# Performance work log

Hardware: AMD Instinct MI355X
Metric: run time of the kernel (lower is better)

Reference implementation:

```python
import jax, jax.numpy as jnp
import numpy as np
from jax import lax

STRIDE = 16
ANCHOR_BASE = 16
PRE_NMS = 6000
POST_NMS = 2000
NMS_THRESH = 0.7


def _generate_anchors(base_size=16, ratios=(0.5, 1.0, 2.0), scales=(8, 16, 32)):
    w = h = float(base_size)
    x_ctr = 0.5 * (w - 1)
    y_ctr = 0.5 * (h - 1)
    size = w * h
    anchors = []
    for r in ratios:
        ws = np.round(np.sqrt(size / r))
        hs = np.round(ws * r)
        for s in scales:
            wss, hss = ws * s, hs * s
            anchors.append([x_ctr - 0.5 * (wss - 1), y_ctr - 0.5 * (hss - 1),
                            x_ctr + 0.5 * (wss - 1), y_ctr + 0.5 * (hss - 1)])
    return np.array(anchors, dtype=np.float32)  # [9,4]


def _all_anchors(width, height, stride):
    base = _generate_anchors(ANCHOR_BASE)  # [A,4]
    sx = np.arange(width, dtype=np.float32) * stride
    gy, gx = np.meshgrid(np.arange(height, dtype=np.float32) * stride, sx, indexing='ij')
    shifts = np.stack([gx.ravel(), gy.ravel(), gx.ravel(), gy.ravel()], axis=1)  # [K,4] h-major
    return jnp.asarray((shifts[:, None, :] + base[None, :, :]).reshape(-1, 4))  # [K*A,4]


def setup_inputs() -> dict:
    key = jax.random.key(0)
    k1, k2 = jax.random.split(key)
    H = W = 64
    bbox_deltas = jax.random.normal(k1, (1, 36, H, W), dtype=jnp.float32)
    scores = jax.random.uniform(k2, (1, 2, 9 * H, W), dtype=jnp.float32)
    return {"bbox_deltas": bbox_deltas, "scores": scores, "im_w": 1024, "im_h": 1024}


def reference(bbox_deltas, scores, im_w, im_h):
    H, W = bbox_deltas.shape[2], bbox_deltas.shape[3]
    # fg scores: reshape [1,2,9H,W] -> [1,18,H,W], take channels 9:18
    sc = scores.reshape(1, 18, H, W)[:, 9:, :, :].transpose(0, 2, 3, 1).reshape(-1)
    dl = bbox_deltas.transpose(0, 2, 3, 1).reshape(-1, 4)
    anchors = _all_anchors(W, H, STRIDE)

    # bbox_transform_inv (decode)
    aw = anchors[:, 2] - anchors[:, 0] + 1.0
    ah = anchors[:, 3] - anchors[:, 1] + 1.0
    acx = anchors[:, 0] + 0.5 * aw
    acy = anchors[:, 1] + 0.5 * ah
    pcx = dl[:, 0] * aw + acx
    pcy = dl[:, 1] * ah + acy
    pw = jnp.exp(dl[:, 2]) * aw
    ph = jnp.exp(dl[:, 3]) * ah
    x1 = jnp.clip(pcx - 0.5 * pw, 0.0, im_w - 1.0)
    y1 = jnp.clip(pcy - 0.5 * ph, 0.0, im_h - 1.0)
    x2 = jnp.clip(pcx + 0.5 * pw, 0.0, im_w - 1.0)
    y2 = jnp.clip(pcy + 0.5 * ph, 0.0, im_h - 1.0)
    props = jnp.stack([x1, y1, x2, y2], axis=1)

    # min-size filter
    thresh = 16.0 * (float(im_h) / float(im_w))
    keep_f = ((x2 - x1 + 1.0) >= thresh) & ((y2 - y1 + 1.0) >= thresh)
    sc_m = jnp.where(keep_f, sc, -jnp.inf)

    # pre-NMS top-k by score
    top_sc, idx = lax.top_k(sc_m, PRE_NMS)
    top_p = props[idx]  # [PRE_NMS,4], sorted by score desc
    valid = jnp.isfinite(top_sc)

    # pairwise IoU (with +1 box convention, as in py_cpu_nms)
    bx1, by1, bx2, by2 = top_p[:, 0], top_p[:, 1], top_p[:, 2], top_p[:, 3]
    areas = (bx2 - bx1 + 1.0) * (by2 - by1 + 1.0)
    iw = jnp.maximum(jnp.minimum(bx2[:, None], bx2[None, :]) - jnp.maximum(bx1[:, None], bx1[None, :]) + 1.0, 0.0)
    ih = jnp.maximum(jnp.minimum(by2[:, None], by2[None, :]) - jnp.maximum(by1[:, None], by1[None, :]) + 1.0, 0.0)
    inter = iw * ih
    iou = inter / (areas[:, None] + areas[None, :] - inter)
    sup = iou > NMS_THRESH  # [N,N]

    ar = jnp.arange(PRE_NMS)

    def body(i, keep):
        row = sup[i] & keep[i] & (ar > i)
        return keep & (~row)

    keep = lax.fori_loop(0, PRE_NMS, body, valid)

    # take first POST_NMS kept (in score order), scatter into fixed-size output
    rank = jnp.cumsum(keep.astype(jnp.int32)) - 1
    sel = keep & (rank < POST_NMS)
    dst = jnp.where(sel, rank, POST_NMS)  # invalid rows dumped into slot POST_NMS
    out_b = jnp.zeros((POST_NMS + 1, 4), dtype=jnp.float32).at[dst].set(
        jnp.where(sel[:, None], top_p, 0.0))[:POST_NMS]
    out_s = jnp.zeros((POST_NMS + 1,), dtype=jnp.float32).at[dst].set(
        jnp.where(sel, top_sc, 0.0))[:POST_NMS]
    blob = jnp.concatenate([jnp.zeros((POST_NMS, 1), dtype=jnp.float32), out_b], axis=1)
    return blob, out_s[:, None]
```

## Files before the change

kernel.cpp:

```cpp
#include <hip/hip_runtime.h>
#include <math.h>

typedef unsigned int u32;
typedef unsigned long long u64;

#define NANCH   36864
#define PRE     6000
#define POST    2000
#define NWORDS  94

#define OFF_PROPS   ((size_t)0)
#define OFF_SV      ((size_t)589824)
#define OFF_SORTED  ((size_t)884736)
#define OFF_SEL     ((size_t)932864)
#define OFF_MASK    ((size_t)1227776)
#define OFF_CTRL    ((size_t)5739776)
#define OFF_H1      ((size_t)5740032)
#define OFF_INVALW  ((size_t)5744384)
#define OFF_KEEPW   ((size_t)5745152)
#define ZERO_BYTES  ((size_t)(256 + 4352 + 768))

__device__ __constant__ float BA[9][4] = {
  {-84.f,-40.f,99.f,55.f},   {-176.f,-88.f,191.f,103.f}, {-360.f,-184.f,375.f,199.f},
  {-56.f,-56.f,71.f,71.f},   {-120.f,-120.f,135.f,135.f},{-248.f,-248.f,263.f,263.f},
  {-36.f,-80.f,51.f,95.f},   {-80.f,-168.f,95.f,183.f},  {-168.f,-344.f,183.f,359.f}};

__device__ __forceinline__ u32 key_bin(u32 key) {
  if (key < 0xBF000000u) return 0u;
  u32 b = ((key >> 13) - 0x5F800u) + 1u;
  return b > 1024u ? 1024u : b;
}

__global__ void decode_k(const float* __restrict__ deltas, const float* __restrict__ scores,
                         const int* __restrict__ imw_p, const int* __restrict__ imh_p,
                         float4* __restrict__ props, u64* __restrict__ sortvals,
                         u32* __restrict__ h1) {
  #pragma clang fp contract(off)
  int i = blockIdx.x * 256 + threadIdx.x;
  if (i >= NANCH) return;
  int a = i % 9;
  int pix = i / 9;
  int x = pix & 63, y = pix >> 6;

  float sc = scores[(9 + a) * 4096 + pix];
  float d0 = deltas[(a * 4 + 0) * 4096 + pix];
  float d1 = deltas[(a * 4 + 1) * 4096 + pix];
  float d2 = deltas[(a * 4 + 2) * 4096 + pix];
  float d3 = deltas[(a * 4 + 3) * 4096 + pix];

  float gx = (float)(x * 16), gy = (float)(y * 16);
  float ax1 = gx + BA[a][0], ay1 = gy + BA[a][1];
  float ax2 = gx + BA[a][2], ay2 = gy + BA[a][3];
  float aw = ax2 - ax1 + 1.0f, ah = ay2 - ay1 + 1.0f;
  float acx = ax1 + 0.5f * aw, acy = ay1 + 0.5f * ah;

  float pcx = d0 * aw + acx;
  float pcy = d1 * ah + acy;
  float pw = (float)exp((double)d2) * aw;
  float ph = (float)exp((double)d3) * ah;

  float imw1 = (float)imw_p[0] - 1.0f, imh1 = (float)imh_p[0] - 1.0f;
  float x1 = fminf(fmaxf(pcx - 0.5f * pw, 0.0f), imw1);
  float y1 = fminf(fmaxf(pcy - 0.5f * ph, 0.0f), imh1);
  float x2 = fminf(fmaxf(pcx + 0.5f * pw, 0.0f), imw1);
  float y2 = fminf(fmaxf(pcy + 0.5f * ph, 0.0f), imh1);
  props[i] = make_float4(x1, y1, x2, y2);

  float thresh = 16.0f * ((float)imh_p[0] / (float)imw_p[0]);
  bool keep = (x2 - x1 + 1.0f >= thresh) && (y2 - y1 + 1.0f >= thresh);
  u32 key = keep ? (__float_as_uint(sc) | 0x80000000u) : 0u;
  sortvals[i] = ((u64)key << 32) | (u64)(0xFFFFFFFFu - (u32)i);
  u32 bin = key_bin(key);
  if (bin) atomicAdd(&h1[bin], 1u);
}

__global__ void scan_k(const u32* __restrict__ h1, u32* __restrict__ ctrl) {
  int l = threadIdx.x;
  u32 loc[16], suf[16];
  #pragma unroll
  for (int k = 0; k < 16; ++k) loc[k] = h1[1 + l * 16 + k];
  u32 acc = 0;
  #pragma unroll
  for (int k = 15; k >= 0; --k) { acc += loc[k]; suf[k] = acc; }
  u32 sfx = acc;
  for (int off = 1; off < 64; off <<= 1) {
    u32 o = __shfl_down(sfx, off);
    if (l + off < 64) sfx += o;
  }
  u32 S_above = sfx - acc;
  u64 mball = __ballot(suf[0] + S_above >= (u32)PRE);
  if (mball == 0ULL) { if (l == 0) ctrl[0] = 0u; return; }
  int L = 63 - __builtin_clzll(mball);
  if (l == L) {
    int kk = 0;
    for (int k = 15; k >= 0; --k)
      if (suf[k] + S_above >= (u32)PRE) { kk = k; break; }
    ctrl[0] = (u32)(1 + 16 * L + kk);
  }
}

__global__ void compact_k(const u64* __restrict__ sv, u32* __restrict__ ctrl,
                          u64* __restrict__ sel) {
  int i = blockIdx.x * 256 + threadIdx.x;
  if (i >= NANCH) return;
  u32 chosen = ctrl[0];
  u64 v = sv[i];
  if (key_bin((u32)(v >> 32)) >= chosen) {
    u32 p = atomicAdd(&ctrl[6], 1u);
    sel[p] = v;
  }
}

__global__ void rank_k(const u64* __restrict__ sel, const u32* __restrict__ ctrl,
                       u64* __restrict__ sorted, u64* __restrict__ invalw) {
  __shared__ u64 sj[256];
  u32 n = ctrl[6];
  int i = blockIdx.x * 256 + threadIdx.x;
  if ((u32)(blockIdx.x * 256) >= n) return;
  u64 vi = ((u32)i < n) ? sel[i] : 0ULL;
  u32 cnt = 0;
  for (u32 jb = 0; jb < n; jb += 256) {
    __syncthreads();
    if (jb + threadIdx.x < n) sj[threadIdx.x] = sel[jb + threadIdx.x];
    __syncthreads();
    u32 m = min(256u, n - jb);
    #pragma unroll 8
    for (u32 j = 0; j < m; ++j) cnt += (u32)(sj[j] > vi);
  }
  if ((u32)i < n && cnt < (u32)PRE) {
    sorted[cnt] = vi;
    if ((u32)(vi >> 32) == 0u)
      atomicOr((unsigned long long*)&invalw[cnt >> 6], 1ULL << (cnt & 63));
  }
}

__global__ void mask_k(const u64* __restrict__ sorted, const float4* __restrict__ props,
                       u64* __restrict__ mask) {
  #pragma clang fp contract(off)
  __shared__ float4 cb[64];
  int jb = blockIdx.x;
  if (jb < (int)blockIdx.y) return;
  int i = blockIdx.y * 64 + threadIdx.x;
  int jj = jb * 64 + threadIdx.x;
  float4 cc = make_float4(0.f, 0.f, 0.f, 0.f);
  if (jj < PRE) {
    u64 v = sorted[jj];
    cc = props[0xFFFFu - ((u32)v & 0xFFFFu)];
  }
  cb[threadIdx.x] = cc;
  __syncthreads();
  if (i >= PRE) return;
  u64 vi = sorted[i];
  float4 b = props[0xFFFFu - ((u32)vi & 0xFFFFu)];
  float ai = (b.z - b.x + 1.0f) * (b.w - b.y + 1.0f);
  u64 bits = 0ULL;
  int jmax = min(64, PRE - jb * 64);
  for (int j = 0; j < jmax; ++j) {
    float4 c = cb[j];
    float aj = (c.z - c.x + 1.0f) * (c.w - c.y + 1.0f);
    float iw = fmaxf(fminf(b.z, c.z) - fmaxf(b.x, c.x) + 1.0f, 0.0f);
    float ih = fmaxf(fminf(b.w, c.w) - fmaxf(b.y, c.y) + 1.0f, 0.0f);
    float inter = iw * ih;
    float iou = inter / (ai + aj - inter);
    bits |= ((u64)(iou > 0.7f)) << j;
  }
  mask[(size_t)i * NWORDS + jb] = bits;
}

__device__ __forceinline__ u64 rl64(u64 v, int lane) {
  u32 lo = (u32)__builtin_amdgcn_readlane((int)(u32)v, lane);
  u32 hi = (u32)__builtin_amdgcn_readlane((int)(u32)(v >> 32), lane);
  return ((u64)hi << 32) | (u64)lo;
}
__device__ __forceinline__ u64 rfl64(u64 v) {
  u32 lo = (u32)__builtin_amdgcn_readfirstlane((int)(u32)v);
  u32 hi = (u32)__builtin_amdgcn_readfirstlane((int)(u32)(v >> 32));
  return ((u64)hi << 32) | (u64)lo;
}

__global__ void __launch_bounds__(1024) nms_scan_k(const u64* __restrict__ mask,
                                                   const u64* __restrict__ invalw,
                                                   u64* __restrict__ keepw) {
  __shared__ u64 Lrem[NWORDS];
  __shared__ u64 Ldiag[64];
  __shared__ u64 Lkeep;
  __shared__ int Lstop;
  __shared__ int Llast;
  const int t = threadIdx.x;
  const int g = t >> 7;
  const int w = t & 127;
  const bool loader = (w < NWORDS);
  if (t < NWORDS) Lrem[t] = invalw[t];
  if (t == 0) { Lstop = 0; Llast = NWORDS - 1; }
  u64 rv = 0;
  u64 B0[8], B1[8], B2[8];
  int kept = 0;
  __syncthreads();

#define ISSUE(bb, BUF) \
  if ((bb) < NWORDS && loader) { \
    u64 st_ = Lrem[(bb)]; \
    const int row0_ = (bb) * 64 + g * 8; \
    const u64* pp_ = mask + (size_t)row0_ * NWORDS + w; \
    _Pragma("unroll") \
    for (int j = 0; j < 8; ++j) { \
      bool ok_ = (w >= (bb)) && (row0_ + j < PRE) && !((st_ >> (g * 8 + j)) & 1ULL); \
      BUF[j] = ok_ ? pp_[(size_t)j * NWORDS] : 0ULL; \
    } \
  }

#define STEP(bb, BUF) { \
    if (w == (bb)) {                      \
      atomicOr((u32*)&Lrem[(bb)], (u32)rv); \
      atomicOr(((u32*)&Lrem[(bb)]) + 1, (u32)(rv >> 32)); \
      _Pragma("unroll") \
      for (int j = 0; j < 8; ++j) Ldiag[g * 8 + j] = BUF[j]; \
    } \
    if ((bb) + 3 < NWORDS && w == (bb) + 3) {   \
      atomicOr((u32*)&Lrem[(bb) + 3], (u32)rv); \
      atomicOr(((u32*)&Lrem[(bb) + 3]) + 1, (u32)(rv >> 32)); \
    } \
    __syncthreads();                      \
    if (t < 64) { \
      u64 dgl = Ldiag[t]; \
      u64 avail = ~rfl64(Lrem[(bb)]);     \
      u64 kb = 0; \
      while (avail) { \
        int i_ = __builtin_ctzll(avail); \
        kb |= 1ULL << i_; \
        u64 di_ = rl64(dgl, i_); \
        avail &= ~di_ & ~((2ULL << i_) - 1ULL);  \
      } \
      if (t == 0) { \
        keepw[(bb)] = kb; \
        Lkeep = kb; \
        kept += (int)__popcll(kb); \
        if (kept >= POST) { Lstop = 1; Llast = (bb); } \
      } \
    } \
    __syncthreads();                      \
    { \
      u64 kb_ = Lkeep; \
      const int base_ = g * 8; \
      _Pragma("unroll") \
      for (int j = 0; j < 8; ++j) { \
        u64 k_ = (kb_ >> (base_ + j)) & 1ULL; \
        rv |= (0ULL - k_) & BUF[j]; \
      } \
    } \
    ISSUE((bb) + 3, BUF)                  \
    if (Lstop) break; }

  ISSUE(0, B0)
  ISSUE(1, B1)
  ISSUE(2, B2)
  for (int bb = 0; bb < NWORDS; bb += 3) {
    STEP(bb, B0)
    if (bb + 1 < NWORDS) STEP(bb + 1, B1)
    if (bb + 2 < NWORDS) STEP(bb + 2, B2)
  }
#undef ISSUE
#undef STEP

  __syncthreads();
  int last = Llast;
  for (int w2 = t; w2 < NWORDS; w2 += 1024)
    if (w2 > last) keepw[w2] = 0ULL;
}

__global__ void outscatter_k(const u64* __restrict__ keepw, const u64* __restrict__ sorted,
                             const float4* __restrict__ props, float* __restrict__ out) {
  __shared__ u64 wl[NWORDS];
  __shared__ u32 pre[NWORDS];
  int t = threadIdx.x;
  for (int i = t; i < 12000; i += 1024) out[i] = 0.0f;
  if (t < NWORDS) wl[t] = keepw[t];
  __syncthreads();
  if (t == 0) {
    u32 run = 0;
    for (int w = 0; w < NWORDS; ++w) { pre[w] = run; run += (u32)__popcll(wl[w]); }
  }
  __syncthreads();
  for (int i = t; i < PRE; i += 1024) {
    int w = i >> 6;
    u64 word = wl[w];
    if ((word >> (i & 63)) & 1ULL) {
      u32 rank = pre[w] + (u32)__popcll(word & ((1ULL << (i & 63)) - 1ULL));
      if (rank < POST) {
        u64 v = sorted[i];
        float4 b = props[0xFFFFu - ((u32)v & 0xFFFFu)];
        out[rank * 5 + 1] = b.x;
        out[rank * 5 + 2] = b.y;
        out[rank * 5 + 3] = b.z;
        out[rank * 5 + 4] = b.w;
        out[10000 + rank] = __uint_as_float((u32)(v >> 32) & 0x7FFFFFFFu);
      }
    }
  }
}

extern "C" void kernel_launch(void* const* d_in, const int* in_sizes, int n_in,
                              void* d_out, int out_size, void* d_ws, size_t ws_size,
                              hipStream_t stream) {
  const float* deltas = (const float*)d_in[0];
  const float* scores = (const float*)d_in[1];
  const int* imw = (const int*)d_in[2];
  const int* imh = (const int*)d_in[3];
  char* ws = (char*)d_ws;

  float4* props   = (float4*)(ws + OFF_PROPS);
  u64*    svals   = (u64*)(ws + OFF_SV);
  u64*    sorted  = (u64*)(ws + OFF_SORTED);
  u64*    sel     = (u64*)(ws + OFF_SEL);
  u64*    maskb   = (u64*)(ws + OFF_MASK);
  u32*    ctrl    = (u32*)(ws + OFF_CTRL);
  u32*    h1      = (u32*)(ws + OFF_H1);
  u64*    invalw  = (u64*)(ws + OFF_INVALW);
  u64*    keepw   = (u64*)(ws + OFF_KEEPW);

  hipMemsetAsync(ws + OFF_CTRL, 0, ZERO_BYTES, stream);

  decode_k<<<144, 256, 0, stream>>>(deltas, scores, imw, imh, props, svals, h1);
  scan_k<<<1, 64, 0, stream>>>(h1, ctrl);
  compact_k<<<144, 256, 0, stream>>>(svals, ctrl, sel);
  rank_k<<<144, 256, 0, stream>>>(sel, ctrl, sorted, invalw);

  dim3 mgrid(NWORDS, NWORDS);
  mask_k<<<mgrid, 64, 0, stream>>>(sorted, props, maskb);

  nms_scan_k<<<1, 1024, 0, stream>>>(maskb, invalw, keepw);
  outscatter_k<<<1, 1024, 0, stream>>>(keepw, sorted, props, (float*)d_out);
}
```

Measured before the change: 334.6 us.

## Replace single-block NMS scan with multi-block pipelined scan over transposed mask

The mask kernel now writes the IoU suppression bitmask column-major (transposed, padded rows), so each column of 64 boxes is contiguous. The single 1024-thread NMS scan is replaced by 47 single-wavefront blocks, each owning two consecutive 64-box words. Each block prefetches its column of mask words, then spin-waits on keep-words that earlier blocks publish through global memory as a value/complement pair, and ORs in the suppression. The serial dependency shrinks to a cross-block handoff of one word, and the many block-wide barriers go away. The cost is agent-scope polling latency, reliance on all blocks being co-resident, and the loss of the early stop once enough boxes are kept.

```diff
diff --git a/kernel.cpp b/kernel.cpp
--- a/kernel.cpp
+++ b/kernel.cpp
@@ -8,17 +8,20 @@
 #define PRE     6000
 #define POST    2000
 #define NWORDS  94
+#define NST     47
+#define ROWSP   6016
 
 #define OFF_PROPS   ((size_t)0)
 #define OFF_SV      ((size_t)589824)
 #define OFF_SORTED  ((size_t)884736)
 #define OFF_SEL     ((size_t)932864)
-#define OFF_MASK    ((size_t)1227776)
-#define OFF_CTRL    ((size_t)5739776)
-#define OFF_H1      ((size_t)5740032)
-#define OFF_INVALW  ((size_t)5744384)
-#define OFF_KEEPW   ((size_t)5745152)
-#define ZERO_BYTES  ((size_t)(256 + 4352 + 768))
+#define OFF_MASKT   ((size_t)1227776)
+#define OFF_CTRL    ((size_t)5751808)
+#define OFF_H1      ((size_t)5752064)
+#define OFF_INVALW  ((size_t)5756416)
+#define OFF_KBP     ((size_t)5757184)
+#define OFF_KBN     ((size_t)5757952)
+#define ZERO_BYTES  ((size_t)(256 + 4352 + 768 + 768 + 768))
 
 __device__ __constant__ float BA[9][4] = {
   {-84.f,-40.f,99.f,55.f},   {-176.f,-88.f,191.f,103.f}, {-360.f,-184.f,375.f,199.f},
@@ -135,7 +138,7 @@
 }
 
 __global__ void mask_k(const u64* __restrict__ sorted, const float4* __restrict__ props,
-                       u64* __restrict__ mask) {
+                       u64* __restrict__ maskT) {
   #pragma clang fp contract(off)
   __shared__ float4 cb[64];
   int jb = blockIdx.x;
@@ -164,7 +167,7 @@
     float iou = inter / (ai + aj - inter);
     bits |= ((u64)(iou > 0.7f)) << j;
   }
-  mask[(size_t)i * NWORDS + jb] = bits;
+  maskT[(size_t)jb * ROWSP + i] = bits;
 }
 
 __device__ __forceinline__ u64 rl64(u64 v, int lane) {
@@ -172,100 +175,77 @@
   u32 hi = (u32)__builtin_amdgcn_readlane((int)(u32)(v >> 32), lane);
   return ((u64)hi << 32) | (u64)lo;
 }
-__device__ __forceinline__ u64 rfl64(u64 v) {
-  u32 lo = (u32)__builtin_amdgcn_readfirstlane((int)(u32)v);
-  u32 hi = (u32)__builtin_amdgcn_readfirstlane((int)(u32)(v >> 32));
-  return ((u64)hi << 32) | (u64)lo;
-}
-
-__global__ void __launch_bounds__(1024) nms_scan_k(const u64* __restrict__ mask,
-                                                   const u64* __restrict__ invalw,
-                                                   u64* __restrict__ keepw) {
-  __shared__ u64 Lrem[NWORDS];
-  __shared__ u64 Ldiag[64];
-  __shared__ u64 Lkeep;
-  __shared__ int Lstop;
-  __shared__ int Llast;
-  const int t = threadIdx.x;
-  const int g = t >> 7;
-  const int w = t & 127;
-  const bool loader = (w < NWORDS);
-  if (t < NWORDS) Lrem[t] = invalw[t];
-  if (t == 0) { Lstop = 0; Llast = NWORDS - 1; }
-  u64 rv = 0;
-  u64 B0[8], B1[8], B2[8];
-  int kept = 0;
-  __syncthreads();
-
-#define ISSUE(bb, BUF) \
-  if ((bb) < NWORDS && loader) { \
-    u64 st_ = Lrem[(bb)]; \
-    const int row0_ = (bb) * 64 + g * 8; \
-    const u64* pp_ = mask + (size_t)row0_ * NWORDS + w; \
-    _Pragma("unroll") \
-    for (int j = 0; j < 8; ++j) { \
-      bool ok_ = (w >= (bb)) && (row0_ + j < PRE) && !((st_ >> (g * 8 + j)) & 1ULL); \
-      BUF[j] = ok_ ? pp_[(size_t)j * NWORDS] : 0ULL; \
-    } \
-  }
-
-#define STEP(bb, BUF) { \
-    if (w == (bb)) {                      \
-      atomicOr((u32*)&Lrem[(bb)], (u32)rv); \
-      atomicOr(((u32*)&Lrem[(bb)]) + 1, (u32)(rv >> 32)); \
-      _Pragma("unroll") \
-      for (int j = 0; j < 8; ++j) Ldiag[g * 8 + j] = BUF[j]; \
-    } \
-    if ((bb) + 3 < NWORDS && w == (bb) + 3) {   \
-      atomicOr((u32*)&Lrem[(bb) + 3], (u32)rv); \
-      atomicOr(((u32*)&Lrem[(bb) + 3]) + 1, (u32)(rv >> 32)); \
-    } \
-    __syncthreads();                      \
-    if (t < 64) { \
-      u64 dgl = Ldiag[t]; \
-      u64 avail = ~rfl64(Lrem[(bb)]);     \
-      u64 kb = 0; \
-      while (avail) { \
-        int i_ = __builtin_ctzll(avail); \
-        kb |= 1ULL << i_; \
-        u64 di_ = rl64(dgl, i_); \
-        avail &= ~di_ & ~((2ULL << i_) - 1ULL);  \
-      } \
-      if (t == 0) { \
-        keepw[(bb)] = kb; \
-        Lkeep = kb; \
-        kept += (int)__popcll(kb); \
-        if (kept >= POST) { Lstop = 1; Llast = (bb); } \
-      } \
-    } \
-    __syncthreads();                      \
-    { \
-      u64 kb_ = Lkeep; \
-      const int base_ = g * 8; \
-      _Pragma("unroll") \
-      for (int j = 0; j < 8; ++j) { \
-        u64 k_ = (kb_ >> (base_ + j)) & 1ULL; \
-        rv |= (0ULL - k_) & BUF[j]; \
-      } \
-    } \
-    ISSUE((bb) + 3, BUF)                  \
-    if (Lstop) break; }
-
-  ISSUE(0, B0)
-  ISSUE(1, B1)
-  ISSUE(2, B2)
-  for (int bb = 0; bb < NWORDS; bb += 3) {
-    STEP(bb, B0)
-    if (bb + 1 < NWORDS) STEP(bb + 1, B1)
-    if (bb + 2 < NWORDS) STEP(bb + 2, B2)
-  }
-#undef ISSUE
-#undef STEP
-
-  __syncthreads();
-  int last = Llast;
-  for (int w2 = t; w2 < NWORDS; w2 += 1024)
-    if (w2 > last) keepw[w2] = 0ULL;
+
+__global__ void __launch_bounds__(64) nms_pipe_k(const u64* __restrict__ maskT,
+                                                 const u64* __restrict__ invalw,
+                                                 u64* kbP, u64* kbN) {
+  const int s = blockIdx.x;
+  const int j = threadIdx.x;
+  const int A = 2 * s, B = A + 1;
+  const u64* colA = maskT + (size_t)A * ROWSP;
+  const u64* colB = maskT + (size_t)B * ROWSP;
+  u64 dA0 = colA[A * 64 + j];
+  u64 dB0 = colB[A * 64 + j];
+  u64 dB1 = colB[B * 64 + j];
+  u64 ivA = invalw[A], ivB = invalw[B];
+  u64 partA = 0, partB = 0;
+  const int P = A;
+  u64 rA[8], rB[8];
+
+  for (int g0 = 0; g0 < P; g0 += 8) {
+    const int gn = min(8, P - g0);
+    #pragma unroll
+    for (int k = 0; k < 8; ++k)
+      if (k < gn) {
+        rA[k] = colA[(g0 + k) * 64 + j];
+        rB[k] = colB[(g0 + k) * 64 + j];
+      }
+    #pragma unroll
+    for (int k = 0; k < 8; ++k)
+      if (k < gn) {
+        const int w = g0 + k;
+        u64 p, q;
+        int spins = 0;
+        do {
+          p = __hip_atomic_load(&kbP[w], __ATOMIC_RELAXED, __HIP_MEMORY_SCOPE_AGENT);
+          q = __hip_atomic_load(&kbN[w], __ATOMIC_RELAXED, __HIP_MEMORY_SCOPE_AGENT);
+        } while (p != ~q && ++spins < 2000000);
+        u64 m = 0ULL - ((p >> j) & 1ULL);
+        partA |= m & rA[k];
+        partB |= m & rB[k];
+      }
+  }
+
+  #pragma unroll
+  for (int off = 1; off < 64; off <<= 1) {
+    partA |= (u64)__shfl_xor((long long)partA, off, 64);
+    partB |= (u64)__shfl_xor((long long)partB, off, 64);
+  }
+  u64 availA = ~(partA | ivA);
+  u64 availB = ~(partB | ivB);
+  if (B == NWORDS - 1) availB &= (1ULL << (PRE - (NWORDS - 1) * 64)) - 1ULL;
+
+  u64 kbA = 0;
+  while (availA) {
+    int i = __builtin_ctzll(availA);
+    kbA |= 1ULL << i;
+    availA &= ~rl64(dA0, i) & ~((2ULL << i) - 1ULL);
+    availB &= ~rl64(dB0, i);
+  }
+  if (j == 0) {
+    __hip_atomic_store(&kbP[A], kbA, __ATOMIC_RELAXED, __HIP_MEMORY_SCOPE_AGENT);
+    __hip_atomic_store(&kbN[A], ~kbA, __ATOMIC_RELAXED, __HIP_MEMORY_SCOPE_AGENT);
+  }
+  u64 kbB = 0;
+  while (availB) {
+    int i = __builtin_ctzll(availB);
+    kbB |= 1ULL << i;
+    availB &= ~rl64(dB1, i) & ~((2ULL << i) - 1ULL);
+  }
+  if (j == 0) {
+    __hip_atomic_store(&kbP[B], kbB, __ATOMIC_RELAXED, __HIP_MEMORY_SCOPE_AGENT);
+    __hip_atomic_store(&kbN[B], ~kbB, __ATOMIC_RELAXED, __HIP_MEMORY_SCOPE_AGENT);
+  }
 }
 
 __global__ void outscatter_k(const u64* __restrict__ keepw, const u64* __restrict__ sorted,
@@ -312,11 +292,12 @@
   u64*    svals   = (u64*)(ws + OFF_SV);
   u64*    sorted  = (u64*)(ws + OFF_SORTED);
   u64*    sel     = (u64*)(ws + OFF_SEL);
-  u64*    maskb   = (u64*)(ws + OFF_MASK);
+  u64*    maskT   = (u64*)(ws + OFF_MASKT);
   u32*    ctrl    = (u32*)(ws + OFF_CTRL);
   u32*    h1      = (u32*)(ws + OFF_H1);
   u64*    invalw  = (u64*)(ws + OFF_INVALW);
-  u64*    keepw   = (u64*)(ws + OFF_KEEPW);
+  u64*    kbP     = (u64*)(ws + OFF_KBP);
+  u64*    kbN     = (u64*)(ws + OFF_KBN);
 
   hipMemsetAsync(ws + OFF_CTRL, 0, ZERO_BYTES, stream);
 
@@ -326,8 +307,8 @@
   rank_k<<<144, 256, 0, stream>>>(sel, ctrl, sorted, invalw);
 
   dim3 mgrid(NWORDS, NWORDS);
-  mask_k<<<mgrid, 64, 0, stream>>>(sorted, props, maskb);
-
-  nms_scan_k<<<1, 1024, 0, stream>>>(maskb, invalw, keepw);
-  outscatter_k<<<1, 1024, 0, stream>>>(keepw, sorted, props, (float*)d_out);
-}
+  mask_k<<<mgrid, 64, 0, stream>>>(sorted, props, maskT);
+
+  nms_pipe_k<<<NST, 64, 0, stream>>>(maskT, invalw, kbP, kbN);
+  outscatter_k<<<1, 1024, 0, stream>>>(kbP, sorted, props, (float*)d_out);
+}
```

Result: slower. 478.4 us (+43.0%).

## Transpose NMS mask, process two words per step, fuse scan/compact and scatter kernels

Applied to the files above, without the earlier changes.

Stores the IoU suppression mask column-major (word-major, padded rows) so the serial NMS kernel reads contiguous 16-row chunks per thread, and the scan now resolves two 64-bit words per barrier step, halving the number of synchronised steps. The histogram threshold scan is folded into compact_k and the output scatter into nms_scan_k, removing two launches. The invalid-row bitmap is built in shared memory rather than with global atomics. The memset is shrunk to the histogram, and ctrl[6] is cleared by decode_k. In exchange the mask loads are no longer skipped for already-suppressed or below-diagonal rows, so the scan reads more mask data. Each step's serial loop is also longer, since it resolves the second word after the first.

```diff
diff --git a/kernel.cpp b/kernel.cpp
--- a/kernel.cpp
+++ b/kernel.cpp
@@ -8,17 +8,16 @@
 #define PRE     6000
 #define POST    2000
 #define NWORDS  94
+#define NSTEP   47
+#define ROWSP   6016
 
 #define OFF_PROPS   ((size_t)0)
 #define OFF_SV      ((size_t)589824)
 #define OFF_SORTED  ((size_t)884736)
 #define OFF_SEL     ((size_t)932864)
-#define OFF_MASK    ((size_t)1227776)
-#define OFF_CTRL    ((size_t)5739776)
-#define OFF_H1      ((size_t)5740032)
-#define OFF_INVALW  ((size_t)5744384)
-#define OFF_KEEPW   ((size_t)5745152)
-#define ZERO_BYTES  ((size_t)(256 + 4352 + 768))
+#define OFF_MASKT   ((size_t)1227776)
+#define OFF_CTRL    ((size_t)5751808)
+#define OFF_H1      ((size_t)5752064)
 
 __device__ __constant__ float BA[9][4] = {
   {-84.f,-40.f,99.f,55.f},   {-176.f,-88.f,191.f,103.f}, {-360.f,-184.f,375.f,199.f},
@@ -34,8 +33,9 @@
 __global__ void decode_k(const float* __restrict__ deltas, const float* __restrict__ scores,
                          const int* __restrict__ imw_p, const int* __restrict__ imh_p,
                          float4* __restrict__ props, u64* __restrict__ sortvals,
-                         u32* __restrict__ h1) {
+                         u32* __restrict__ h1, u32* __restrict__ ctrl) {
   #pragma clang fp contract(off)
+  if (threadIdx.x == 0) ctrl[6] = 0u;
   int i = blockIdx.x * 256 + threadIdx.x;
   if (i >= NANCH) return;
   int a = i % 9;
@@ -74,36 +74,40 @@
   if (bin) atomicAdd(&h1[bin], 1u);
 }
 
-__global__ void scan_k(const u32* __restrict__ h1, u32* __restrict__ ctrl) {
-  int l = threadIdx.x;
-  u32 loc[16], suf[16];
-  #pragma unroll
-  for (int k = 0; k < 16; ++k) loc[k] = h1[1 + l * 16 + k];
-  u32 acc = 0;
-  #pragma unroll
-  for (int k = 15; k >= 0; --k) { acc += loc[k]; suf[k] = acc; }
-  u32 sfx = acc;
-  for (int off = 1; off < 64; off <<= 1) {
-    u32 o = __shfl_down(sfx, off);
-    if (l + off < 64) sfx += o;
-  }
-  u32 S_above = sfx - acc;
-  u64 mball = __ballot(suf[0] + S_above >= (u32)PRE);
-  if (mball == 0ULL) { if (l == 0) ctrl[0] = 0u; return; }
-  int L = 63 - __builtin_clzll(mball);
-  if (l == L) {
-    int kk = 0;
-    for (int k = 15; k >= 0; --k)
-      if (suf[k] + S_above >= (u32)PRE) { kk = k; break; }
-    ctrl[0] = (u32)(1 + 16 * L + kk);
-  }
-}
-
-__global__ void compact_k(const u64* __restrict__ sv, u32* __restrict__ ctrl,
-                          u64* __restrict__ sel) {
-  int i = blockIdx.x * 256 + threadIdx.x;
+__global__ void compact_k(const u64* __restrict__ sv, const u32* __restrict__ h1,
+                          u32* __restrict__ ctrl, u64* __restrict__ sel) {
+  __shared__ u32 Lchosen;
+  int t = threadIdx.x;
+  if (t < 64) {
+    int l = t;
+    u32 loc[16], suf[16];
+    #pragma unroll
+    for (int k = 0; k < 16; ++k) loc[k] = h1[1 + l * 16 + k];
+    u32 acc = 0;
+    #pragma unroll
+    for (int k = 15; k >= 0; --k) { acc += loc[k]; suf[k] = acc; }
+    u32 sfx = acc;
+    for (int off = 1; off < 64; off <<= 1) {
+      u32 o = __shfl_down(sfx, off);
+      if (l + off < 64) sfx += o;
+    }
+    u32 S_above = sfx - acc;
+    u64 mball = __ballot(suf[0] + S_above >= (u32)PRE);
+    if (mball == 0ULL) { if (l == 0) Lchosen = 0u; }
+    else {
+      int L = 63 - __builtin_clzll(mball);
+      if (l == L) {
+        int kk = 0;
+        for (int k = 15; k >= 0; --k)
+          if (suf[k] + S_above >= (u32)PRE) { kk = k; break; }
+        Lchosen = (u32)(1 + 16 * L + kk);
+      }
+    }
+  }
+  __syncthreads();
+  u32 chosen = Lchosen;
+  int i = blockIdx.x * 256 + t;
   if (i >= NANCH) return;
-  u32 chosen = ctrl[0];
   u64 v = sv[i];
   if (key_bin((u32)(v >> 32)) >= chosen) {
     u32 p = atomicAdd(&ctrl[6], 1u);
@@ -112,7 +116,7 @@
 }
 
 __global__ void rank_k(const u64* __restrict__ sel, const u32* __restrict__ ctrl,
-                       u64* __restrict__ sorted, u64* __restrict__ invalw) {
+                       u64* __restrict__ sorted) {
   __shared__ u64 sj[256];
   u32 n = ctrl[6];
   int i = blockIdx.x * 256 + threadIdx.x;
@@ -127,15 +131,11 @@
     #pragma unroll 8
     for (u32 j = 0; j < m; ++j) cnt += (u32)(sj[j] > vi);
   }
-  if ((u32)i < n && cnt < (u32)PRE) {
-    sorted[cnt] = vi;
-    if ((u32)(vi >> 32) == 0u)
-      atomicOr((unsigned long long*)&invalw[cnt >> 6], 1ULL << (cnt & 63));
-  }
+  if ((u32)i < n && cnt < (u32)PRE) sorted[cnt] = vi;
 }
 
 __global__ void mask_k(const u64* __restrict__ sorted, const float4* __restrict__ props,
-                       u64* __restrict__ mask) {
+                       u64* __restrict__ maskT) {
   #pragma clang fp contract(off)
   __shared__ float4 cb[64];
   int jb = blockIdx.x;
@@ -164,7 +164,7 @@
     float iou = inter / (ai + aj - inter);
     bits |= ((u64)(iou > 0.7f)) << j;
   }
-  mask[(size_t)i * NWORDS + jb] = bits;
+  maskT[(size_t)jb * ROWSP + i] = bits;
 }
 
 __device__ __forceinline__ u64 rl64(u64 v, int lane) {
@@ -172,120 +172,112 @@
   u32 hi = (u32)__builtin_amdgcn_readlane((int)(u32)(v >> 32), lane);
   return ((u64)hi << 32) | (u64)lo;
 }
-__device__ __forceinline__ u64 rfl64(u64 v) {
-  u32 lo = (u32)__builtin_amdgcn_readfirstlane((int)(u32)v);
-  u32 hi = (u32)__builtin_amdgcn_readfirstlane((int)(u32)(v >> 32));
-  return ((u64)hi << 32) | (u64)lo;
-}
-
-__global__ void __launch_bounds__(1024) nms_scan_k(const u64* __restrict__ mask,
-                                                   const u64* __restrict__ invalw,
-                                                   u64* __restrict__ keepw) {
+
+__global__ void __launch_bounds__(1024) nms_scan_k(const u64* __restrict__ maskT,
+                                                   const u64* __restrict__ sorted,
+                                                   const float4* __restrict__ props,
+                                                   float* __restrict__ out) {
   __shared__ u64 Lrem[NWORDS];
-  __shared__ u64 Ldiag[64];
-  __shared__ u64 Lkeep;
+  __shared__ u64 Ldiag[128][2];
+  __shared__ u64 Lkb[NWORDS];
+  __shared__ u64 LkA, LkB;
   __shared__ int Lstop;
-  __shared__ int Llast;
+  __shared__ u32 Lpre[NWORDS];
   const int t = threadIdx.x;
   const int g = t >> 7;
   const int w = t & 127;
   const bool loader = (w < NWORDS);
-  if (t < NWORDS) Lrem[t] = invalw[t];
-  if (t == 0) { Lstop = 0; Llast = NWORDS - 1; }
   u64 rv = 0;
-  u64 B0[8], B1[8], B2[8];
+  u64 B0[16], B1[16];
   int kept = 0;
-  __syncthreads();
 
 #define ISSUE(bb, BUF) \
-  if ((bb) < NWORDS && loader) { \
-    u64 st_ = Lrem[(bb)]; \
-    const int row0_ = (bb) * 64 + g * 8; \
-    const u64* pp_ = mask + (size_t)row0_ * NWORDS + w; \
+  if ((bb) < NSTEP && loader) { \
+    const u64* p_ = maskT + (size_t)w * ROWSP + (bb) * 128 + g * 16; \
     _Pragma("unroll") \
-    for (int j = 0; j < 8; ++j) { \
-      bool ok_ = (w >= (bb)) && (row0_ + j < PRE) && !((st_ >> (g * 8 + j)) & 1ULL); \
-      BUF[j] = ok_ ? pp_[(size_t)j * NWORDS] : 0ULL; \
-    } \
-  }
+    for (int k = 0; k < 16; ++k) BUF[k] = p_[k]; \
+  }
+
+  ISSUE(0, B0)
+  ISSUE(1, B1)
+
+  if (t < NWORDS) { Lrem[t] = 0ULL; Lkb[t] = 0ULL; }
+  if (t == 0) Lstop = 0;
+  __syncthreads();
+  for (int r = t; r < PRE; r += 1024)
+    if ((u32)(sorted[r] >> 32) == 0u)
+      atomicOr((unsigned long long*)&Lrem[r >> 6], 1ULL << (r & 63));
+  if (t == 0)
+    atomicOr((unsigned long long*)&Lrem[NWORDS - 1],
+             ~((1ULL << (PRE - (NWORDS - 1) * 64)) - 1ULL));
+  __syncthreads();
 
 #define STEP(bb, BUF) { \
-    if (w == (bb)) {                      \
-      atomicOr((u32*)&Lrem[(bb)], (u32)rv); \
-      atomicOr(((u32*)&Lrem[(bb)]) + 1, (u32)(rv >> 32)); \
+    const int A_ = 2 * (bb), Bw_ = A_ + 1; \
+    if (w == A_ || w == Bw_) {            \
+      atomicOr((u32*)&Lrem[w], (u32)rv); \
+      atomicOr(((u32*)&Lrem[w]) + 1, (u32)(rv >> 32)); \
+      const int c_ = (w == Bw_); \
       _Pragma("unroll") \
-      for (int j = 0; j < 8; ++j) Ldiag[g * 8 + j] = BUF[j]; \
-    } \
-    if ((bb) + 3 < NWORDS && w == (bb) + 3) {   \
-      atomicOr((u32*)&Lrem[(bb) + 3], (u32)rv); \
-      atomicOr(((u32*)&Lrem[(bb) + 3]) + 1, (u32)(rv >> 32)); \
+      for (int k = 0; k < 16; ++k) { \
+        int i_ = g * 16 + k; \
+        if (c_ || i_ < 64) Ldiag[i_][c_] = BUF[k]; \
+      } \
     } \
     __syncthreads();                      \
     if (t < 64) { \
-      u64 dgl = Ldiag[t]; \
-      u64 avail = ~rfl64(Lrem[(bb)]);     \
-      u64 kb = 0; \
-      while (avail) { \
-        int i_ = __builtin_ctzll(avail); \
-        kb |= 1ULL << i_; \
-        u64 di_ = rl64(dgl, i_); \
-        avail &= ~di_ & ~((2ULL << i_) - 1ULL);  \
+      u64 a0 = Ldiag[t][0], b0 = Ldiag[t][1], b1 = Ldiag[64 + t][1]; \
+      u64 availA = ~Lrem[A_]; \
+      u64 availB = ~Lrem[Bw_]; \
+      u64 kbA = 0, kbB = 0; \
+      while (availA) { \
+        int i_ = __builtin_ctzll(availA); \
+        kbA |= 1ULL << i_; \
+        availA &= ~rl64(a0, i_) & ~((2ULL << i_) - 1ULL);  \
+        availB &= ~rl64(b0, i_); \
+      } \
+      while (availB) { \
+        int i_ = __builtin_ctzll(availB); \
+        kbB |= 1ULL << i_; \
+        availB &= ~rl64(b1, i_) & ~((2ULL << i_) - 1ULL); \
       } \
       if (t == 0) { \
-        keepw[(bb)] = kb; \
-        Lkeep = kb; \
-        kept += (int)__popcll(kb); \
-        if (kept >= POST) { Lstop = 1; Llast = (bb); } \
+        Lkb[A_] = kbA; Lkb[Bw_] = kbB; LkA = kbA; LkB = kbB; \
+        kept += (int)__popcll(kbA) + (int)__popcll(kbB); \
+        if (kept >= POST) Lstop = 1; \
       } \
     } \
     __syncthreads();                      \
     { \
-      u64 kb_ = Lkeep; \
-      const int base_ = g * 8; \
+      u64 kA_ = LkA, kB_ = LkB; \
       _Pragma("unroll") \
-      for (int j = 0; j < 8; ++j) { \
-        u64 k_ = (kb_ >> (base_ + j)) & 1ULL; \
-        rv |= (0ULL - k_) & BUF[j]; \
+      for (int k = 0; k < 16; ++k) { \
+        int i_ = g * 16 + k; \
+        u64 bit_ = (i_ < 64) ? (kA_ >> i_) : (kB_ >> (i_ - 64)); \
+        rv |= (0ULL - (bit_ & 1ULL)) & BUF[k]; \
       } \
     } \
-    ISSUE((bb) + 3, BUF)                  \
+    ISSUE((bb) + 2, BUF)                  \
     if (Lstop) break; }
 
-  ISSUE(0, B0)
-  ISSUE(1, B1)
-  ISSUE(2, B2)
-  for (int bb = 0; bb < NWORDS; bb += 3) {
+  for (int bb = 0; bb < NSTEP; bb += 2) {
     STEP(bb, B0)
-    if (bb + 1 < NWORDS) STEP(bb + 1, B1)
-    if (bb + 2 < NWORDS) STEP(bb + 2, B2)
+    if (bb + 1 < NSTEP) STEP(bb + 1, B1)
   }
 #undef ISSUE
 #undef STEP
 
   __syncthreads();
-  int last = Llast;
-  for (int w2 = t; w2 < NWORDS; w2 += 1024)
-    if (w2 > last) keepw[w2] = 0ULL;
-}
-
-__global__ void outscatter_k(const u64* __restrict__ keepw, const u64* __restrict__ sorted,
-                             const float4* __restrict__ props, float* __restrict__ out) {
-  __shared__ u64 wl[NWORDS];
-  __shared__ u32 pre[NWORDS];
-  int t = threadIdx.x;
   for (int i = t; i < 12000; i += 1024) out[i] = 0.0f;
-  if (t < NWORDS) wl[t] = keepw[t];
-  __syncthreads();
   if (t == 0) {
     u32 run = 0;
-    for (int w = 0; w < NWORDS; ++w) { pre[w] = run; run += (u32)__popcll(wl[w]); }
+    for (int w2 = 0; w2 < NWORDS; ++w2) { Lpre[w2] = run; run += (u32)__popcll(Lkb[w2]); }
   }
   __syncthreads();
   for (int i = t; i < PRE; i += 1024) {
-    int w = i >> 6;
-    u64 word = wl[w];
+    u64 word = Lkb[i >> 6];
     if ((word >> (i & 63)) & 1ULL) {
-      u32 rank = pre[w] + (u32)__popcll(word & ((1ULL << (i & 63)) - 1ULL));
+      u32 rank = Lpre[i >> 6] + (u32)__popcll(word & ((1ULL << (i & 63)) - 1ULL));
       if (rank < POST) {
         u64 v = sorted[i];
         float4 b = props[0xFFFFu - ((u32)v & 0xFFFFu)];
@@ -312,22 +304,18 @@
   u64*    svals   = (u64*)(ws + OFF_SV);
   u64*    sorted  = (u64*)(ws + OFF_SORTED);
   u64*    sel     = (u64*)(ws + OFF_SEL);
-  u64*    maskb   = (u64*)(ws + OFF_MASK);
+  u64*    maskT   = (u64*)(ws + OFF_MASKT);
   u32*    ctrl    = (u32*)(ws + OFF_CTRL);
   u32*    h1      = (u32*)(ws + OFF_H1);
-  u64*    invalw  = (u64*)(ws + OFF_INVALW);
-  u64*    keepw   = (u64*)(ws + OFF_KEEPW);
-
-  hipMemsetAsync(ws + OFF_CTRL, 0, ZERO_BYTES, stream);
-
-  decode_k<<<144, 256, 0, stream>>>(deltas, scores, imw, imh, props, svals, h1);
-  scan_k<<<1, 64, 0, stream>>>(h1, ctrl);
-  compact_k<<<144, 256, 0, stream>>>(svals, ctrl, sel);
-  rank_k<<<144, 256, 0, stream>>>(sel, ctrl, sorted, invalw);
+
+  hipMemsetAsync(h1, 0, 1025 * sizeof(u32), stream);
+
+  decode_k<<<144, 256, 0, stream>>>(deltas, scores, imw, imh, props, svals, h1, ctrl);
+  compact_k<<<144, 256, 0, stream>>>(svals, h1, ctrl, sel);
+  rank_k<<<144, 256, 0, stream>>>(sel, ctrl, sorted);
 
   dim3 mgrid(NWORDS, NWORDS);
-  mask_k<<<mgrid, 64, 0, stream>>>(sorted, props, maskb);
-
-  nms_scan_k<<<1, 1024, 0, stream>>>(maskb, invalw, keepw);
-  outscatter_k<<<1, 1024, 0, stream>>>(keepw, sorted, props, (float*)d_out);
-}
+  mask_k<<<mgrid, 64, 0, stream>>>(sorted, props, maskT);
+
+  nms_scan_k<<<1, 1024, 0, stream>>>(maskT, sorted, props, (float*)d_out);
+}
```

New measurement: 378.8 us. 1.13x slower.
